# Performance work log

Hardware: AMD Instinct MI355X
Metric: run time of the kernel (lower is better)

## Reference

```python
import jax, jax.numpy as jnp
import numpy as np

N = 50000          # total nodes
B = 10             # graphs in batch
NPG = N // B       # nodes per graph (equal-sized graphs)
E = 800000         # edges
IN_DIM = 128
HID = 128
NHEAD = 4
DHEAD = HID // NHEAD
T = 1000
SLOPE = 0.2        # leaky_relu negative slope
ALPHA_L = 2.0


def _ln(x, g=None, b=None, eps=1e-5):
    mu = jnp.mean(x, axis=-1, keepdims=True)
    var = jnp.var(x, axis=-1, keepdims=True)
    y = (x - mu) * jax.lax.rsqrt(var + eps)
    if g is not None:
        y = y * g + b
    return y


def _gatv2(h, src, dst, Ws, Wd, a, b):
    # DGL GATv2Conv, share_weights=False, residual=False, bias=True, activation=gelu
    fs = (h @ Ws).reshape(N, NHEAD, DHEAD)
    fd = (h @ Wd).reshape(N, NHEAD, DHEAD)
    # per-edge attention logits [E, NHEAD]
    e = jnp.sum(jax.nn.leaky_relu(fs[src] + fd[dst], SLOPE) * a, axis=-1)
    # edge softmax grouped by destination node
    m = jax.ops.segment_max(e, dst, num_segments=N)
    ee = jnp.exp(e - m[dst])
    den = jax.ops.segment_sum(ee, dst, num_segments=N)
    alpha = ee / den[dst]                                  # [E, NHEAD]
    rst = jax.ops.segment_sum(alpha[..., None] * fs[src], dst, num_segments=N)
    rst = jax.nn.gelu(rst + b.reshape(1, NHEAD, DHEAD), approximate=False)
    return rst.reshape(N, HID)


def _forward(x, noise, sab, somab, time_emb,
             Ws0, Wd0, a0, b0, g0, be0,
             Ws1, Wd1, a1, b1, g1, be1,
             Wo1, bo1, Wo2, bo2, src, dst, t):
    # sample_q: statistics-matched signed noise
    miu = jnp.mean(x, axis=0)
    std = jnp.std(x, axis=0, ddof=1)          # torch.std is unbiased
    nz = _ln(noise) * std + miu
    nz = jnp.sign(x) * jnp.abs(nz)
    s1 = jnp.repeat(sab[t], NPG)[:, None]
    s2 = jnp.repeat(somab[t], NPG)[:, None]
    x_t = s1 * x + s2 * nz
    temb = jnp.repeat(time_emb[t], NPG, axis=0)
    # Denoising_Unet
    h = jnp.concatenate([x_t, temb], axis=1)   # [N, IN_DIM+HID]
    h = _ln(_gatv2(h, src, dst, Ws0, Wd0, a0, b0), g0, be0)
    h_in = h
    h = _gatv2(h, src, dst, Ws1, Wd1, a1, b1)
    h = _ln(h + h_in, g1, be1)                 # residual (shapes match)
    out = jax.nn.relu(h @ Wo1 + bo1) @ Wo2 + bo2
    # loss_fn
    mse = jnp.mean((out - x) ** 2)
    on = out / jnp.maximum(jnp.linalg.norm(out, axis=-1, keepdims=True), 1e-12)
    xn = x / jnp.maximum(jnp.linalg.norm(x, axis=-1, keepdims=True), 1e-12)
    cos = jnp.mean((1.0 - jnp.sum(on * xn, axis=-1)) ** ALPHA_L)
    return mse + 0.1 * cos


def setup_inputs() -> dict:
    key = jax.random.key(0)
    ks = jax.random.split(key, 26)
    betas = np.linspace(1e-4, 0.02, T, dtype=np.float64)
    ab = np.cumprod(1.0 - betas)
    s = 0.02
    in0 = IN_DIM + HID
    inp = {}
    inp['x'] = jax.random.normal(ks[0], (N, IN_DIM), jnp.float32)
    inp['noise'] = jax.random.normal(ks[1], (N, IN_DIM), jnp.float32)
    inp['src'] = jax.random.randint(ks[2], (E,), 0, N, dtype=jnp.int32)
    inp['dst'] = jax.random.randint(ks[3], (E,), 0, N, dtype=jnp.int32)
    inp['t'] = jax.random.randint(ks[4], (B,), 0, T, dtype=jnp.int32)
    inp['sab'] = jnp.asarray(np.sqrt(ab), jnp.float32)
    inp['somab'] = jnp.asarray(np.sqrt(1.0 - ab), jnp.float32)
    inp['time_emb'] = jax.random.normal(ks[5], (T, HID), jnp.float32) * s
    inp['Ws0'] = jax.random.normal(ks[6], (in0, HID), jnp.float32) * s
    inp['Wd0'] = jax.random.normal(ks[7], (in0, HID), jnp.float32) * s
    inp['a0'] = jax.random.normal(ks[8], (NHEAD, DHEAD), jnp.float32) * s
    inp['b0'] = jnp.zeros((HID,), jnp.float32)
    inp['g0'] = jnp.ones((HID,), jnp.float32)
    inp['be0'] = jnp.zeros((HID,), jnp.float32)
    inp['Ws1'] = jax.random.normal(ks[9], (HID, HID), jnp.float32) * s
    inp['Wd1'] = jax.random.normal(ks[10], (HID, HID), jnp.float32) * s
    inp['a1'] = jax.random.normal(ks[11], (NHEAD, DHEAD), jnp.float32) * s
    inp['b1'] = jnp.zeros((HID,), jnp.float32)
    inp['g1'] = jnp.ones((HID,), jnp.float32)
    inp['be1'] = jnp.zeros((HID,), jnp.float32)
    inp['Wo1'] = jax.random.normal(ks[12], (HID, HID), jnp.float32) * s
    inp['bo1'] = jnp.zeros((HID,), jnp.float32)
    inp['Wo2'] = jax.random.normal(ks[13], (HID, IN_DIM), jnp.float32) * s
    inp['bo2'] = jnp.zeros((IN_DIM,), jnp.float32)
    return inp


def reference(x, noise, src, dst, t, sab, somab, time_emb,
              Ws0, Wd0, a0, b0, g0, be0,
              Ws1, Wd1, a1, b1, g1, be1,
              Wo1, bo1, Wo2, bo2):
    return _forward(x, noise, sab, somab, time_emb,
                    Ws0, Wd0, a0, b0, g0, be0,
                    Ws1, Wd1, a1, b1, g1, be1,
                    Wo1, bo1, Wo2, bo2, src, dst, t)
```

## Files before the change

### kernel.cpp

```cpp
#include <hip/hip_runtime.h>
#include <hip/hip_bf16.h>
#include <math.h>

#define NN 50000
#define EE 800000
#define NPG 5000

typedef short bf16x8 __attribute__((ext_vector_type(8)));
typedef float f32x4 __attribute__((ext_vector_type(4)));

__device__ __forceinline__ float gelu_exact(float v) {
    return 0.5f * v * (1.0f + erff(v * 0.70710678118654752440f));
}

__device__ __forceinline__ ushort f2b(float f) {
    union { float f; uint u; } v; v.f = f;
    uint r = (v.u + 0x7fffu + ((v.u >> 16) & 1)) >> 16;
    return (ushort)r;
}
__device__ __forceinline__ uint pack2(float a, float b) {
    return (uint)f2b(a) | ((uint)f2b(b) << 16);
}
__device__ __forceinline__ float blo(uint u) {
    union { uint u; float f; } v; v.u = u << 16; return v.f;
}
__device__ __forceinline__ float bhi(uint u) {
    union { uint u; float f; } v; v.u = u & 0xffff0000u; return v.f;
}

__global__ void probe_kernel(int* sink) {
    if (blockIdx.x == 99999) sink[0] = 1;
}

__global__ __launch_bounds__(256) void colstats_kernel(const float* __restrict__ x,
                                                       float* __restrict__ sums, int n) {
    int tid = threadIdx.x;
    int col4 = (tid & 31) * 4;
    int rowgrp = tid >> 5;
    float s0 = 0.f, s1 = 0.f, s2 = 0.f, s3 = 0.f;
    float q0 = 0.f, q1 = 0.f, q2 = 0.f, q3 = 0.f;
    for (int r = blockIdx.x * 8 + rowgrp; r < n; r += gridDim.x * 8) {
        float4 v = *(const float4*)(x + (size_t)r * 128 + col4);
        s0 += v.x; s1 += v.y; s2 += v.z; s3 += v.w;
        q0 += v.x * v.x; q1 += v.y * v.y; q2 += v.z * v.z; q3 += v.w * v.w;
    }
    s0 += __shfl_xor(s0, 32); s1 += __shfl_xor(s1, 32);
    s2 += __shfl_xor(s2, 32); s3 += __shfl_xor(s3, 32);
    q0 += __shfl_xor(q0, 32); q1 += __shfl_xor(q1, 32);
    q2 += __shfl_xor(q2, 32); q3 += __shfl_xor(q3, 32);
    __shared__ float red[4][32][8];
    int wv = tid >> 6, l = tid & 63;
    if (l < 32) {
        float* p = red[wv][l];
        p[0] = s0; p[1] = s1; p[2] = s2; p[3] = s3;
        p[4] = q0; p[5] = q1; p[6] = q2; p[7] = q3;
    }
    __syncthreads();
    if (tid < 32) {
        float a0 = 0.f, a1 = 0.f, a2 = 0.f, a3 = 0.f;
        float b0 = 0.f, b1 = 0.f, b2 = 0.f, b3 = 0.f;
#pragma unroll
        for (int w = 0; w < 4; ++w) {
            float* p = red[w][tid];
            a0 += p[0]; a1 += p[1]; a2 += p[2]; a3 += p[3];
            b0 += p[4]; b1 += p[5]; b2 += p[6]; b3 += p[7];
        }
        int c = tid * 4;
        atomicAdd(&sums[c], a0); atomicAdd(&sums[c + 1], a1);
        atomicAdd(&sums[c + 2], a2); atomicAdd(&sums[c + 3], a3);
        atomicAdd(&sums[128 + c], b0); atomicAdd(&sums[128 + c + 1], b1);
        atomicAdd(&sums[128 + c + 2], b2); atomicAdd(&sums[128 + c + 3], b3);
    }
}

__global__ void finalize_stats_kernel(float* __restrict__ stats, int n) {
    int c = threadIdx.x;
    float sum = stats[c], sumsq = stats[128 + c];
    float mu = sum / (float)n;
    float var = (sumsq - sum * sum / (float)n) / (float)(n - 1);
    stats[256 + c] = mu;
    stats[384 + c] = sqrtf(fmaxf(var, 0.f));
}

__global__ __launch_bounds__(256) void build_h_kernel(const float* __restrict__ x,
        const float* __restrict__ noise, const int* __restrict__ t,
        const float* __restrict__ sab, const float* __restrict__ somab,
        const float* __restrict__ temb, const float* __restrict__ stats,
        ushort* __restrict__ h, int n) {
    int wid = (blockIdx.x * blockDim.x + threadIdx.x) >> 6;
    int lane = threadIdx.x & 63;
    if (wid >= n) return;
    int tt = t[wid / NPG];
    float s1 = sab[tt], s2v = somab[tt];
    float2 nz = ((const float2*)noise)[(size_t)wid * 64 + lane];
    float s = nz.x + nz.y;
    float sq = nz.x * nz.x + nz.y * nz.y;
#pragma unroll
    for (int o = 1; o < 64; o <<= 1) { s += __shfl_xor(s, o); sq += __shfl_xor(sq, o); }
    float mu = s * (1.f / 128.f);
    float var = sq * (1.f / 128.f) - mu * mu;
    float r = rsqrtf(var + 1e-5f);
    int f0 = 2 * lane, f1 = f0 + 1;
    float y0 = (nz.x - mu) * r * stats[384 + f0] + stats[256 + f0];
    float y1 = (nz.y - mu) * r * stats[384 + f1] + stats[256 + f1];
    float2 xv = ((const float2*)x)[(size_t)wid * 64 + lane];
    float sg0 = (xv.x > 0.f) ? 1.f : ((xv.x < 0.f) ? -1.f : 0.f);
    float sg1 = (xv.y > 0.f) ? 1.f : ((xv.y < 0.f) ? -1.f : 0.f);
    float n0 = sg0 * fabsf(y0);
    float n1 = sg1 * fabsf(y1);
    float xt0 = s1 * xv.x + s2v * n0;
    float xt1 = s1 * xv.y + s2v * n1;
    uint* row = (uint*)(h + (size_t)wid * 256);
    row[lane] = pack2(xt0, xt1);
    float2 te = ((const float2*)(temb + (size_t)tt * 128))[lane];
    row[64 + lane] = pack2(te.x, te.y);
}

__global__ __launch_bounds__(256) void convert_weights(const float* __restrict__ Ws0,
        const float* __restrict__ Wd0, const float* __restrict__ Ws1,
        const float* __restrict__ Wd1, const float* __restrict__ Wo1,
        const float* __restrict__ Wo2, ushort* __restrict__ Wt0,
        ushort* __restrict__ Wt1, ushort* __restrict__ Wo1t, ushort* __restrict__ Wo2t) {
    int i = blockIdx.x * 256 + threadIdx.x;
    if (i < 65536) {
        int c = i >> 8, k = i & 255;
        const float* W = (c < 128) ? Ws0 : Wd0;
        Wt0[c * 256 + k] = f2b(W[k * 128 + (c & 127)]);
    } else if (i < 98304) {
        int j = i - 65536;
        int c = j >> 7, k = j & 127;
        const float* W = (c < 128) ? Ws1 : Wd1;
        Wt1[c * 128 + k] = f2b(W[k * 128 + (c & 127)]);
    } else if (i < 114688) {
        int j = i - 98304;
        int c = j >> 7, k = j & 127;
        Wo1t[c * 128 + k] = f2b(Wo1[k * 128 + c]);
    } else if (i < 131072) {
        int j = i - 114688;
        int c = j >> 7, k = j & 127;
        Wo2t[c * 128 + k] = f2b(Wo2[k * 128 + c]);
    }
}

__global__ void hist_kernel(const int* __restrict__ dst, int* __restrict__ counts, int e) {
    int i = blockIdx.x * blockDim.x + threadIdx.x;
    if (i < e) atomicAdd(&counts[dst[i]], 1);
}

__global__ __launch_bounds__(1024) void scan_reduce_kernel(const int* __restrict__ counts,
        int* __restrict__ blockSums, int n) {
    int i = blockIdx.x * 1024 + threadIdx.x;
    int v = (i < n) ? counts[i] : 0;
#pragma unroll
    for (int o = 32; o > 0; o >>= 1) v += __shfl_down(v, o);
    __shared__ int sh[16];
    int lane = threadIdx.x & 63, wv = threadIdx.x >> 6;
    if (lane == 0) sh[wv] = v;
    __syncthreads();
    if (threadIdx.x == 0) {
        int s = 0;
#pragma unroll
        for (int k = 0; k < 16; ++k) s += sh[k];
        blockSums[blockIdx.x] = s;
    }
}

__global__ __launch_bounds__(64) void scan_offsets_kernel(const int* __restrict__ blockSums,
        int* __restrict__ blockOffs, int* __restrict__ indptr, int nb, int n) {
    int tid = threadIdx.x;
    int v = (tid < nb) ? blockSums[tid] : 0;
    int incl = v;
#pragma unroll
    for (int o = 1; o < 64; o <<= 1) {
        int tv = __shfl_up(incl, o);
        if (tid >= o) incl += tv;
    }
    if (tid < nb) blockOffs[tid] = incl - v;
    if (tid == 63) indptr[n] = incl;
}

__global__ __launch_bounds__(1024) void scan_apply_kernel(const int* __restrict__ counts,
        const int* __restrict__ blockOffs, int* __restrict__ indptr,
        int* __restrict__ cursor, int n) {
    int tid = threadIdx.x;
    int i = blockIdx.x * 1024 + tid;
    int v = (i < n) ? counts[i] : 0;
    int lane = tid & 63, wv = tid >> 6;
    int incl = v;
#pragma unroll
    for (int o = 1; o < 64; o <<= 1) {
        int tv = __shfl_up(incl, o);
        if (lane >= o) incl += tv;
    }
    __shared__ int wsum[16];
    __shared__ int woff[16];
    if (lane == 63) wsum[wv] = incl;
    __syncthreads();
    if (tid == 0) {
        int s = 0;
#pragma unroll
        for (int k = 0; k < 16; ++k) { woff[k] = s; s += wsum[k]; }
    }
    __syncthreads();
    int ex = incl - v + woff[wv] + blockOffs[blockIdx.x];
    if (i < n) { indptr[i] = ex; cursor[i] = ex; }
}

__global__ void scatter_kernel(const int* __restrict__ src, const int* __restrict__ dst,
                               int* __restrict__ cursor, int* __restrict__ csr_src, int e) {
    int i = blockIdx.x * blockDim.x + threadIdx.x;
    if (i < e) {
        int p = atomicAdd(&cursor[dst[i]], 1);
        csr_src[p] = src[i];
    }
}

template<int K, int EPI>
__global__ __launch_bounds__(256, 2) void gemm_resW(const ushort* __restrict__ A,
        const ushort* __restrict__ Wt, const float* __restrict__ bias,
        ushort* __restrict__ C0, float* __restrict__ Cf, int M) {
    constexpr int K2 = K * 2;
    __shared__ ushort Wl[128 * K];
    int tid = threadIdx.x;
    int wave = tid >> 6, lane = tid & 63;
    int l15 = lane & 15, g = lane >> 4;

#pragma unroll
    for (int it = 0; it < K / 16; ++it) {
        int q = (it * 256 + tid) * 16;
        int col = q / K2, qk = q % K2;
        int srcb = col * K2 + (qk ^ ((col & 7) << 4));
        *(float4*)((char*)Wl + q) = *(const float4*)((const char*)Wt + srcb);
    }
    __syncthreads();

    int rowBase = blockIdx.x * 256 + wave * 64;
    f32x4 acc[4][8] = {};

#pragma unroll
    for (int ks = 0; ks < K / 32; ++ks) {
        bf16x8 af[4];
#pragma unroll
        for (int fr = 0; fr < 4; ++fr) {
            int row = rowBase + fr * 16 + l15;
            int rc = min(row, M - 1);
            af[fr] = *(const bf16x8*)(A + (size_t)rc * K + ks * 32 + g * 8);
        }
#pragma unroll
        for (int n = 0; n < 8; ++n) {
            int col = n * 16 + l15;
            int boff = col * K2 + (((ks * 64 + g * 16)) ^ ((col & 7) << 4));
            bf16x8 bf = *(const bf16x8*)((const char*)Wl + boff);
#pragma unroll
            for (int fr = 0; fr < 4; ++fr)
                acc[fr][n] = __builtin_amdgcn_mfma_f32_16x16x32_bf16(af[fr], bf, acc[fr][n], 0, 0, 0);
        }
    }

#pragma unroll
    for (int fr = 0; fr < 4; ++fr) {
#pragma unroll
        for (int n = 0; n < 8; ++n) {
            int col = n * 16 + l15;
#pragma unroll
            for (int j = 0; j < 4; ++j) {
                int row = rowBase + fr * 16 + g * 4 + j;
                if (row < M) {
                    float v = acc[fr][n][j];
                    if (EPI == 1) v = fmaxf(v + bias[col], 0.f);
                    if (EPI == 2) v = v + bias[col];
                    if (EPI == 2) Cf[(size_t)row * 128 + col] = v;
                    else          C0[(size_t)row * 128 + col] = f2b(v);
                }
            }
        }
    }
}

__global__ __launch_bounds__(256) void gat_ln_kernel(const ushort* __restrict__ fs,
        const ushort* __restrict__ fd, const float* __restrict__ a,
        const float* __restrict__ bias, const int* __restrict__ indptr,
        const int* __restrict__ csr_src, const float* __restrict__ resid,
        const float* __restrict__ g, const float* __restrict__ be,
        float* __restrict__ outF, ushort* __restrict__ outB, int n) {
    int wid = (blockIdx.x * blockDim.x + threadIdx.x) >> 6;
    int lane = threadIdx.x & 63;
    if (wid >= n) return;
    int beg = indptr[wid], cnt = indptr[wid + 1] - beg;
    const int* ip = csr_src + beg;
    uint fdu = ((const uint*)fd)[(size_t)wid * 64 + lane];
    float fd0 = blo(fdu), fd1 = bhi(fdu);
    float a0 = a[2 * lane], a1 = a[2 * lane + 1];
    const uint* fsu = (const uint*)fs;
    float den = 0.f, acc0 = 0.f, acc1 = 0.f;
    int s0 = (0 < cnt) ? ip[0] : 0;
    int s1 = (1 < cnt) ? ip[1] : 0;
    int s2 = (2 < cnt) ? ip[2] : 0;
    int s3 = (3 < cnt) ? ip[3] : 0;
    uint v0 = fsu[(size_t)s0 * 64 + lane];
    uint v1 = fsu[(size_t)s1 * 64 + lane];
    uint v2 = fsu[(size_t)s2 * 64 + lane];
    uint v3 = fsu[(size_t)s3 * 64 + lane];
    int i0 = (4 < cnt) ? ip[4] : 0;
    int i1 = (5 < cnt) ? ip[5] : 0;
    int i2 = (6 < cnt) ? ip[6] : 0;
    int i3 = (7 < cnt) ? ip[7] : 0;
    for (int j = 0; j < cnt; ++j) {
        uint cur = v0;
        v0 = v1; v1 = v2; v2 = v3;
        v3 = fsu[(size_t)i0 * 64 + lane];
        i0 = i1; i1 = i2; i2 = i3;
        i3 = (j + 8 < cnt) ? ip[j + 8] : 0;
        float c0 = blo(cur), c1 = bhi(cur);
        float t0 = c0 + fd0; t0 = (t0 > 0.f ? t0 : 0.2f * t0) * a0;
        float t1 = c1 + fd1; t1 = (t1 > 0.f ? t1 : 0.2f * t1) * a1;
        float p = t0 + t1;
        p += __shfl_xor(p, 1); p += __shfl_xor(p, 2);
        p += __shfl_xor(p, 4); p += __shfl_xor(p, 8);
        float w = __expf(p);
        den += w;
        acc0 = fmaf(w, c0, acc0);
        acc1 = fmaf(w, c1, acc1);
    }
    float inv = (cnt > 0) ? 1.f / den : 0.f;
    float r0 = gelu_exact(acc0 * inv + bias[2 * lane]);
    float r1 = gelu_exact(acc1 * inv + bias[2 * lane + 1]);
    if (resid) {
        float2 rr = ((const float2*)resid)[(size_t)wid * 64 + lane];
        r0 += rr.x; r1 += rr.y;
    }
    float s = r0 + r1;
    float sq = r0 * r0 + r1 * r1;
#pragma unroll
    for (int o = 1; o < 64; o <<= 1) { s += __shfl_xor(s, o); sq += __shfl_xor(sq, o); }
    float mu = s * (1.f / 128.f);
    float var = sq * (1.f / 128.f) - mu * mu;
    float rstd = rsqrtf(var + 1e-5f);
    float2 gg = ((const float2*)g)[lane];
    float2 bb = ((const float2*)be)[lane];
    float o0 = (r0 - mu) * rstd * gg.x + bb.x;
    float o1 = (r1 - mu) * rstd * gg.y + bb.y;
    if (outF) ((float2*)outF)[(size_t)wid * 64 + lane] = make_float2(o0, o1);
    if (outB) ((uint*)outB)[(size_t)wid * 64 + lane] = pack2(o0, o1);
}

__global__ __launch_bounds__(256) void loss_partial_kernel(const float* __restrict__ out,
        const float* __restrict__ x, float* __restrict__ partials, int n) {
    __shared__ float sm[8];
    int lane = threadIdx.x & 63;
    int wv = threadIdx.x >> 6;
    int gw = blockIdx.x * 4 + wv;
    float d2 = 0.f, closs = 0.f;
    for (int row = gw; row < n; row += 4096) {
        float2 o = ((const float2*)out)[(size_t)row * 64 + lane];
        float2 xv = ((const float2*)x)[(size_t)row * 64 + lane];
        float e0 = o.x - xv.x, e1 = o.y - xv.y;
        d2 += e0 * e0 + e1 * e1;
        float oo = o.x * o.x + o.y * o.y;
        float xx = xv.x * xv.x + xv.y * xv.y;
        float ox = o.x * xv.x + o.y * xv.y;
#pragma unroll
        for (int s = 1; s < 64; s <<= 1) {
            oo += __shfl_xor(oo, s); xx += __shfl_xor(xx, s); ox += __shfl_xor(ox, s);
        }
        float no = fmaxf(sqrtf(oo), 1e-12f);
        float nx = fmaxf(sqrtf(xx), 1e-12f);
        float cs = 1.f - ox / (no * nx);
        closs += cs * cs;
    }
#pragma unroll
    for (int s = 1; s < 64; s <<= 1) d2 += __shfl_xor(d2, s);
    if (lane == 0) { sm[wv] = d2; sm[4 + wv] = closs; }
    __syncthreads();
    if (threadIdx.x == 0) {
        partials[2 * blockIdx.x] = sm[0] + sm[1] + sm[2] + sm[3];
        partials[2 * blockIdx.x + 1] = sm[4] + sm[5] + sm[6] + sm[7];
    }
}

__global__ __launch_bounds__(1024) void loss_final_kernel(const float* __restrict__ partials,
        float* __restrict__ outp, int nb, int n) {
    __shared__ double sd[32];
    int tid = threadIdx.x;
    double m = 0.0, c = 0.0;
    for (int i = tid; i < nb; i += 1024) { m += partials[2 * i]; c += partials[2 * i + 1]; }
#pragma unroll
    for (int s = 1; s < 64; s <<= 1) { m += __shfl_xor(m, s); c += __shfl_xor(c, s); }
    int wv = tid >> 6, lane = tid & 63;
    if (lane == 0) { sd[wv] = m; sd[16 + wv] = c; }
    __syncthreads();
    if (tid == 0) {
        double mt = 0.0, ct = 0.0;
        for (int i = 0; i < 16; ++i) { mt += sd[i]; ct += sd[16 + i]; }
        outp[0] = (float)(mt / ((double)n * 128.0) + 0.1 * ct / (double)n);
    }
}

extern "C" void kernel_launch(void* const* d_in, const int* in_sizes, int n_in,
                              void* d_out, int out_size, void* d_ws, size_t ws_size,
                              hipStream_t stream) {
    const int N = NN, E = EE;
    const float* x     = (const float*)d_in[0];
    const float* noise = (const float*)d_in[1];
    const int*   src   = (const int*)d_in[2];
    const int*   dst   = (const int*)d_in[3];
    const int*   t     = (const int*)d_in[4];
    const float* sab   = (const float*)d_in[5];
    const float* somab = (const float*)d_in[6];
    const float* temb  = (const float*)d_in[7];
    const float* Ws0   = (const float*)d_in[8];
    const float* Wd0   = (const float*)d_in[9];
    const float* a0    = (const float*)d_in[10];
    const float* b0    = (const float*)d_in[11];
    const float* g0    = (const float*)d_in[12];
    const float* be0   = (const float*)d_in[13];
    const float* Ws1   = (const float*)d_in[14];
    const float* Wd1   = (const float*)d_in[15];
    const float* a1    = (const float*)d_in[16];
    const float* b1    = (const float*)d_in[17];
    const float* g1    = (const float*)d_in[18];
    const float* be1   = (const float*)d_in[19];
    const float* Wo1   = (const float*)d_in[20];
    const float* bo1   = (const float*)d_in[21];
    const float* Wo2   = (const float*)d_in[22];
    const float* bo2   = (const float*)d_in[23];

    float* ws = (float*)d_ws;
    ushort* hB  = (ushort*)ws;
    ushort* Pb  = (ushort*)ws;
    ushort* fsB = (ushort*)(ws + (size_t)N * 128);
    ushort* fdB = (ushort*)(ws + (size_t)N * 192);
    float*  P   = ws + (size_t)N * 256;
    float*  outb = P;
    ushort* Qb  = fdB;
    ushort* z   = fsB;
    float* wtail = ws + (size_t)N * 384;
    ushort* Wt0  = (ushort*)wtail;
    ushort* Wt1  = (ushort*)(wtail + 32768);
    ushort* Wo1t = (ushort*)(wtail + 49152);
    ushort* Wo2t = (ushort*)(wtail + 57344);
    float* stats    = wtail + 65536;
    float* partials = stats + 512;
    int* counts  = (int*)(partials + 2048);
    int* indptr  = counts + N;
    int* cursor  = indptr + N + 1;
    int* csr_src = cursor + N;
    int* blockSums = csr_src + E;
    int* blockOffs = blockSums + 64;

    probe_kernel<<<256, 64, 0, stream>>>(blockSums);

    hipMemsetAsync(stats, 0, 512 * sizeof(float), stream);
    hipMemsetAsync(counts, 0, (size_t)N * sizeof(int), stream);

    colstats_kernel<<<1024, 256, 0, stream>>>(x, stats, N);
    finalize_stats_kernel<<<1, 128, 0, stream>>>(stats, N);
    build_h_kernel<<<(N + 3) / 4, 256, 0, stream>>>(x, noise, t, sab, somab, temb, stats, hB, N);
    convert_weights<<<512, 256, 0, stream>>>(Ws0, Wd0, Ws1, Wd1, Wo1, Wo2, Wt0, Wt1, Wo1t, Wo2t);

    hist_kernel<<<(E + 255) / 256, 256, 0, stream>>>(dst, counts, E);
    int nScanB = (N + 1023) / 1024;
    scan_reduce_kernel<<<nScanB, 1024, 0, stream>>>(counts, blockSums, N);
    scan_offsets_kernel<<<1, 64, 0, stream>>>(blockSums, blockOffs, indptr, nScanB, N);
    scan_apply_kernel<<<nScanB, 1024, 0, stream>>>(counts, blockOffs, indptr, cursor, N);
    scatter_kernel<<<(E + 255) / 256, 256, 0, stream>>>(src, dst, cursor, csr_src, E);

    int gemmGrid = (N + 255) / 256;
    gemm_resW<256, 0><<<gemmGrid, 256, 0, stream>>>(hB, Wt0, nullptr, fsB, nullptr, N);
    gemm_resW<256, 0><<<gemmGrid, 256, 0, stream>>>(hB, Wt0 + 128 * 256, nullptr, fdB, nullptr, N);
    gat_ln_kernel<<<(N + 3) / 4, 256, 0, stream>>>(fsB, fdB, a0, b0, indptr, csr_src,
                                                   nullptr, g0, be0, P, Pb, N);
    gemm_resW<128, 0><<<gemmGrid, 256, 0, stream>>>(Pb, Wt1, nullptr, fsB, nullptr, N);
    gemm_resW<128, 0><<<gemmGrid, 256, 0, stream>>>(Pb, Wt1 + 128 * 128, nullptr, fdB, nullptr, N);
    gat_ln_kernel<<<(N + 3) / 4, 256, 0, stream>>>(fsB, fdB, a1, b1, indptr, csr_src,
                                                   P, g1, be1, nullptr, Qb, N);
    gemm_resW<128, 1><<<gemmGrid, 256, 0, stream>>>(Qb, Wo1t, bo1, z, nullptr, N);
    gemm_resW<128, 2><<<gemmGrid, 256, 0, stream>>>(z, Wo2t, bo2, nullptr, outb, N);

    loss_partial_kernel<<<1024, 256, 0, stream>>>(outb, x, partials, N);
    loss_final_kernel<<<1, 1024, 0, stream>>>(partials, (float*)d_out, 1024, N);
}
```

Measured before the change: 473.7 us.

## Merge preprocessing kernels, batch paired GEMMs, split GAT edges across two waves

Folds column stats, histogram and weight conversion into one launch, then merges the stats finalize with the scan reduce, and the h build with the scan apply. This cuts kernel launches and drops the probe kernel. The fs/fd GEMM pairs now run as one launch each by selecting weights and outputs per block. The GAT aggregation splits each node's edges across two waves with a deeper gather prefetch and combines the partial sums through shared memory. The trade-off is an extra block-wide sync in the GAT kernel and more register pressure from the 8-deep prefetch.

```diff
diff --git a/kernel.cpp b/kernel.cpp
--- a/kernel.cpp
+++ b/kernel.cpp
@@ -28,187 +28,190 @@
     union { uint u; float f; } v; v.u = u & 0xffff0000u; return v.f;
 }
 
-__global__ void probe_kernel(int* sink) {
-    if (blockIdx.x == 99999) sink[0] = 1;
-}
-
-__global__ __launch_bounds__(256) void colstats_kernel(const float* __restrict__ x,
-                                                       float* __restrict__ sums, int n) {
+__global__ __launch_bounds__(256) void head1_kernel(const float* __restrict__ x,
+        float* __restrict__ sums, const int* __restrict__ dst, int* __restrict__ counts,
+        const float* __restrict__ Ws0, const float* __restrict__ Wd0,
+        const float* __restrict__ Ws1, const float* __restrict__ Wd1,
+        const float* __restrict__ Wo1, const float* __restrict__ Wo2,
+        ushort* __restrict__ Wt0, ushort* __restrict__ Wt1,
+        ushort* __restrict__ Wo1t, ushort* __restrict__ Wo2t) {
+    int bid = blockIdx.x;
     int tid = threadIdx.x;
-    int col4 = (tid & 31) * 4;
-    int rowgrp = tid >> 5;
-    float s0 = 0.f, s1 = 0.f, s2 = 0.f, s3 = 0.f;
-    float q0 = 0.f, q1 = 0.f, q2 = 0.f, q3 = 0.f;
-    for (int r = blockIdx.x * 8 + rowgrp; r < n; r += gridDim.x * 8) {
-        float4 v = *(const float4*)(x + (size_t)r * 128 + col4);
-        s0 += v.x; s1 += v.y; s2 += v.z; s3 += v.w;
-        q0 += v.x * v.x; q1 += v.y * v.y; q2 += v.z * v.z; q3 += v.w * v.w;
-    }
-    s0 += __shfl_xor(s0, 32); s1 += __shfl_xor(s1, 32);
-    s2 += __shfl_xor(s2, 32); s3 += __shfl_xor(s3, 32);
-    q0 += __shfl_xor(q0, 32); q1 += __shfl_xor(q1, 32);
-    q2 += __shfl_xor(q2, 32); q3 += __shfl_xor(q3, 32);
-    __shared__ float red[4][32][8];
-    int wv = tid >> 6, l = tid & 63;
-    if (l < 32) {
-        float* p = red[wv][l];
-        p[0] = s0; p[1] = s1; p[2] = s2; p[3] = s3;
-        p[4] = q0; p[5] = q1; p[6] = q2; p[7] = q3;
-    }
-    __syncthreads();
-    if (tid < 32) {
-        float a0 = 0.f, a1 = 0.f, a2 = 0.f, a3 = 0.f;
-        float b0 = 0.f, b1 = 0.f, b2 = 0.f, b3 = 0.f;
-#pragma unroll
-        for (int w = 0; w < 4; ++w) {
-            float* p = red[w][tid];
-            a0 += p[0]; a1 += p[1]; a2 += p[2]; a3 += p[3];
-            b0 += p[4]; b1 += p[5]; b2 += p[6]; b3 += p[7];
-        }
-        int c = tid * 4;
-        atomicAdd(&sums[c], a0); atomicAdd(&sums[c + 1], a1);
-        atomicAdd(&sums[c + 2], a2); atomicAdd(&sums[c + 3], a3);
-        atomicAdd(&sums[128 + c], b0); atomicAdd(&sums[128 + c + 1], b1);
-        atomicAdd(&sums[128 + c + 2], b2); atomicAdd(&sums[128 + c + 3], b3);
-    }
-}
-
-__global__ void finalize_stats_kernel(float* __restrict__ stats, int n) {
-    int c = threadIdx.x;
-    float sum = stats[c], sumsq = stats[128 + c];
-    float mu = sum / (float)n;
-    float var = (sumsq - sum * sum / (float)n) / (float)(n - 1);
-    stats[256 + c] = mu;
-    stats[384 + c] = sqrtf(fmaxf(var, 0.f));
-}
-
-__global__ __launch_bounds__(256) void build_h_kernel(const float* __restrict__ x,
+    if (bid < 1024) {
+        int col4 = (tid & 31) * 4;
+        int rowgrp = tid >> 5;
+        float s0 = 0.f, s1 = 0.f, s2 = 0.f, s3 = 0.f;
+        float q0 = 0.f, q1 = 0.f, q2 = 0.f, q3 = 0.f;
+        for (int r = bid * 8 + rowgrp; r < NN; r += 8192) {
+            float4 v = *(const float4*)(x + (size_t)r * 128 + col4);
+            s0 += v.x; s1 += v.y; s2 += v.z; s3 += v.w;
+            q0 += v.x * v.x; q1 += v.y * v.y; q2 += v.z * v.z; q3 += v.w * v.w;
+        }
+        s0 += __shfl_xor(s0, 32); s1 += __shfl_xor(s1, 32);
+        s2 += __shfl_xor(s2, 32); s3 += __shfl_xor(s3, 32);
+        q0 += __shfl_xor(q0, 32); q1 += __shfl_xor(q1, 32);
+        q2 += __shfl_xor(q2, 32); q3 += __shfl_xor(q3, 32);
+        __shared__ float red[4][32][8];
+        int wv = tid >> 6, l = tid & 63;
+        if (l < 32) {
+            float* p = red[wv][l];
+            p[0] = s0; p[1] = s1; p[2] = s2; p[3] = s3;
+            p[4] = q0; p[5] = q1; p[6] = q2; p[7] = q3;
+        }
+        __syncthreads();
+        if (tid < 32) {
+            float a0 = 0.f, a1 = 0.f, a2 = 0.f, a3 = 0.f;
+            float b0 = 0.f, b1 = 0.f, b2 = 0.f, b3 = 0.f;
+#pragma unroll
+            for (int w = 0; w < 4; ++w) {
+                float* p = red[w][tid];
+                a0 += p[0]; a1 += p[1]; a2 += p[2]; a3 += p[3];
+                b0 += p[4]; b1 += p[5]; b2 += p[6]; b3 += p[7];
+            }
+            int c = tid * 4;
+            atomicAdd(&sums[c], a0); atomicAdd(&sums[c + 1], a1);
+            atomicAdd(&sums[c + 2], a2); atomicAdd(&sums[c + 3], a3);
+            atomicAdd(&sums[128 + c], b0); atomicAdd(&sums[128 + c + 1], b1);
+            atomicAdd(&sums[128 + c + 2], b2); atomicAdd(&sums[128 + c + 3], b3);
+        }
+    } else if (bid < 4149) {
+        int i = (bid - 1024) * 256 + tid;
+        if (i < EE) atomicAdd(&counts[dst[i]], 1);
+    } else {
+        int i = (bid - 4149) * 256 + tid;
+        if (i < 65536) {
+            int c = i >> 8, k = i & 255;
+            const float* W = (c < 128) ? Ws0 : Wd0;
+            Wt0[c * 256 + k] = f2b(W[k * 128 + (c & 127)]);
+        } else if (i < 98304) {
+            int j = i - 65536;
+            int c = j >> 7, k = j & 127;
+            const float* W = (c < 128) ? Ws1 : Wd1;
+            Wt1[c * 128 + k] = f2b(W[k * 128 + (c & 127)]);
+        } else if (i < 114688) {
+            int j = i - 98304;
+            int c = j >> 7, k = j & 127;
+            Wo1t[c * 128 + k] = f2b(Wo1[k * 128 + c]);
+        } else if (i < 131072) {
+            int j = i - 114688;
+            int c = j >> 7, k = j & 127;
+            Wo2t[c * 128 + k] = f2b(Wo2[k * 128 + c]);
+        }
+    }
+}
+
+__global__ __launch_bounds__(1024) void head2_kernel(const int* __restrict__ counts,
+        int* __restrict__ blockSums, float* __restrict__ stats, int n) {
+    int bid = blockIdx.x;
+    int tid = threadIdx.x;
+    if (bid < 49) {
+        int i = bid * 1024 + tid;
+        int v = (i < n) ? counts[i] : 0;
+#pragma unroll
+        for (int o = 32; o > 0; o >>= 1) v += __shfl_down(v, o);
+        __shared__ int sh[16];
+        int lane = tid & 63, wv = tid >> 6;
+        if (lane == 0) sh[wv] = v;
+        __syncthreads();
+        if (tid == 0) {
+            int s = 0;
+#pragma unroll
+            for (int k = 0; k < 16; ++k) s += sh[k];
+            blockSums[bid] = s;
+        }
+    } else {
+        if (tid < 128) {
+            int c = tid;
+            float sum = stats[c], sumsq = stats[128 + c];
+            float mu = sum / (float)n;
+            float var = (sumsq - sum * sum / (float)n) / (float)(n - 1);
+            stats[256 + c] = mu;
+            stats[384 + c] = sqrtf(fmaxf(var, 0.f));
+        }
+    }
+}
+
+__global__ __launch_bounds__(1024) void head3_kernel(const float* __restrict__ x,
         const float* __restrict__ noise, const int* __restrict__ t,
         const float* __restrict__ sab, const float* __restrict__ somab,
         const float* __restrict__ temb, const float* __restrict__ stats,
-        ushort* __restrict__ h, int n) {
-    int wid = (blockIdx.x * blockDim.x + threadIdx.x) >> 6;
-    int lane = threadIdx.x & 63;
-    if (wid >= n) return;
-    int tt = t[wid / NPG];
-    float s1 = sab[tt], s2v = somab[tt];
-    float2 nz = ((const float2*)noise)[(size_t)wid * 64 + lane];
-    float s = nz.x + nz.y;
-    float sq = nz.x * nz.x + nz.y * nz.y;
-#pragma unroll
-    for (int o = 1; o < 64; o <<= 1) { s += __shfl_xor(s, o); sq += __shfl_xor(sq, o); }
-    float mu = s * (1.f / 128.f);
-    float var = sq * (1.f / 128.f) - mu * mu;
-    float r = rsqrtf(var + 1e-5f);
-    int f0 = 2 * lane, f1 = f0 + 1;
-    float y0 = (nz.x - mu) * r * stats[384 + f0] + stats[256 + f0];
-    float y1 = (nz.y - mu) * r * stats[384 + f1] + stats[256 + f1];
-    float2 xv = ((const float2*)x)[(size_t)wid * 64 + lane];
-    float sg0 = (xv.x > 0.f) ? 1.f : ((xv.x < 0.f) ? -1.f : 0.f);
-    float sg1 = (xv.y > 0.f) ? 1.f : ((xv.y < 0.f) ? -1.f : 0.f);
-    float n0 = sg0 * fabsf(y0);
-    float n1 = sg1 * fabsf(y1);
-    float xt0 = s1 * xv.x + s2v * n0;
-    float xt1 = s1 * xv.y + s2v * n1;
-    uint* row = (uint*)(h + (size_t)wid * 256);
-    row[lane] = pack2(xt0, xt1);
-    float2 te = ((const float2*)(temb + (size_t)tt * 128))[lane];
-    row[64 + lane] = pack2(te.x, te.y);
-}
-
-__global__ __launch_bounds__(256) void convert_weights(const float* __restrict__ Ws0,
-        const float* __restrict__ Wd0, const float* __restrict__ Ws1,
-        const float* __restrict__ Wd1, const float* __restrict__ Wo1,
-        const float* __restrict__ Wo2, ushort* __restrict__ Wt0,
-        ushort* __restrict__ Wt1, ushort* __restrict__ Wo1t, ushort* __restrict__ Wo2t) {
-    int i = blockIdx.x * 256 + threadIdx.x;
-    if (i < 65536) {
-        int c = i >> 8, k = i & 255;
-        const float* W = (c < 128) ? Ws0 : Wd0;
-        Wt0[c * 256 + k] = f2b(W[k * 128 + (c & 127)]);
-    } else if (i < 98304) {
-        int j = i - 65536;
-        int c = j >> 7, k = j & 127;
-        const float* W = (c < 128) ? Ws1 : Wd1;
-        Wt1[c * 128 + k] = f2b(W[k * 128 + (c & 127)]);
-    } else if (i < 114688) {
-        int j = i - 98304;
-        int c = j >> 7, k = j & 127;
-        Wo1t[c * 128 + k] = f2b(Wo1[k * 128 + c]);
-    } else if (i < 131072) {
-        int j = i - 114688;
-        int c = j >> 7, k = j & 127;
-        Wo2t[c * 128 + k] = f2b(Wo2[k * 128 + c]);
-    }
-}
-
-__global__ void hist_kernel(const int* __restrict__ dst, int* __restrict__ counts, int e) {
-    int i = blockIdx.x * blockDim.x + threadIdx.x;
-    if (i < e) atomicAdd(&counts[dst[i]], 1);
-}
-
-__global__ __launch_bounds__(1024) void scan_reduce_kernel(const int* __restrict__ counts,
-        int* __restrict__ blockSums, int n) {
+        ushort* __restrict__ h,
+        const int* __restrict__ counts, const int* __restrict__ blockSums,
+        int* __restrict__ indptr, int* __restrict__ cursor, int n) {
+    int bid = blockIdx.x;
+    int tid = threadIdx.x;
+    if (bid < 3125) {
+        int wid = bid * 16 + (tid >> 6);
+        int lane = tid & 63;
+        int tt = t[wid / NPG];
+        float s1 = sab[tt], s2v = somab[tt];
+        float2 nz = ((const float2*)noise)[(size_t)wid * 64 + lane];
+        float s = nz.x + nz.y;
+        float sq = nz.x * nz.x + nz.y * nz.y;
+#pragma unroll
+        for (int o = 1; o < 64; o <<= 1) { s += __shfl_xor(s, o); sq += __shfl_xor(sq, o); }
+        float mu = s * (1.f / 128.f);
+        float var = sq * (1.f / 128.f) - mu * mu;
+        float r = rsqrtf(var + 1e-5f);
+        int f0 = 2 * lane, f1 = f0 + 1;
+        float y0 = (nz.x - mu) * r * stats[384 + f0] + stats[256 + f0];
+        float y1 = (nz.y - mu) * r * stats[384 + f1] + stats[256 + f1];
+        float2 xv = ((const float2*)x)[(size_t)wid * 64 + lane];
+        float sg0 = (xv.x > 0.f) ? 1.f : ((xv.x < 0.f) ? -1.f : 0.f);
+        float sg1 = (xv.y > 0.f) ? 1.f : ((xv.y < 0.f) ? -1.f : 0.f);
+        float n0 = sg0 * fabsf(y0);
+        float n1 = sg1 * fabsf(y1);
+        float xt0 = s1 * xv.x + s2v * n0;
+        float xt1 = s1 * xv.y + s2v * n1;
+        uint* row = (uint*)(h + (size_t)wid * 256);
+        row[lane] = pack2(xt0, xt1);
+        float2 te = ((const float2*)(temb + (size_t)tt * 128))[lane];
+        row[64 + lane] = pack2(te.x, te.y);
+    } else {
+        int b = bid - 3125;
+        __shared__ int sOff, sTot;
+        if (tid < 64) {
+            int v = (tid < 49) ? blockSums[tid] : 0;
+            int incl = v;
+#pragma unroll
+            for (int o = 1; o < 64; o <<= 1) {
+                int tv = __shfl_up(incl, o);
+                if ((tid & 63) >= o) incl += tv;
+            }
+            int off = (b == 0) ? 0 : __shfl(incl, b - 1);
+            int tot = __shfl(incl, 48);
+            if (tid == 0) { sOff = off; sTot = tot; }
+        }
+        __syncthreads();
+        int i = b * 1024 + tid;
+        int v = (i < n) ? counts[i] : 0;
+        int lane = tid & 63, wv = tid >> 6;
+        int incl = v;
+#pragma unroll
+        for (int o = 1; o < 64; o <<= 1) {
+            int tv = __shfl_up(incl, o);
+            if (lane >= o) incl += tv;
+        }
+        __shared__ int wsum[16];
+        __shared__ int woff[16];
+        if (lane == 63) wsum[wv] = incl;
+        __syncthreads();
+        if (tid == 0) {
+            int s = 0;
+#pragma unroll
+            for (int k = 0; k < 16; ++k) { woff[k] = s; s += wsum[k]; }
+        }
+        __syncthreads();
+        int ex = incl - v + woff[wv] + sOff;
+        if (i < n) { indptr[i] = ex; cursor[i] = ex; }
+        if (b == 48 && tid == 0) indptr[n] = sTot;
+    }
+}
+
+__global__ __launch_bounds__(1024) void scatter_kernel(const int* __restrict__ src,
+        const int* __restrict__ dst, int* __restrict__ cursor,
+        int* __restrict__ csr_src, int e) {
     int i = blockIdx.x * 1024 + threadIdx.x;
-    int v = (i < n) ? counts[i] : 0;
-#pragma unroll
-    for (int o = 32; o > 0; o >>= 1) v += __shfl_down(v, o);
-    __shared__ int sh[16];
-    int lane = threadIdx.x & 63, wv = threadIdx.x >> 6;
-    if (lane == 0) sh[wv] = v;
-    __syncthreads();
-    if (threadIdx.x == 0) {
-        int s = 0;
-#pragma unroll
-        for (int k = 0; k < 16; ++k) s += sh[k];
-        blockSums[blockIdx.x] = s;
-    }
-}
-
-__global__ __launch_bounds__(64) void scan_offsets_kernel(const int* __restrict__ blockSums,
-        int* __restrict__ blockOffs, int* __restrict__ indptr, int nb, int n) {
-    int tid = threadIdx.x;
-    int v = (tid < nb) ? blockSums[tid] : 0;
-    int incl = v;
-#pragma unroll
-    for (int o = 1; o < 64; o <<= 1) {
-        int tv = __shfl_up(incl, o);
-        if (tid >= o) incl += tv;
-    }
-    if (tid < nb) blockOffs[tid] = incl - v;
-    if (tid == 63) indptr[n] = incl;
-}
-
-__global__ __launch_bounds__(1024) void scan_apply_kernel(const int* __restrict__ counts,
-        const int* __restrict__ blockOffs, int* __restrict__ indptr,
-        int* __restrict__ cursor, int n) {
-    int tid = threadIdx.x;
-    int i = blockIdx.x * 1024 + tid;
-    int v = (i < n) ? counts[i] : 0;
-    int lane = tid & 63, wv = tid >> 6;
-    int incl = v;
-#pragma unroll
-    for (int o = 1; o < 64; o <<= 1) {
-        int tv = __shfl_up(incl, o);
-        if (lane >= o) incl += tv;
-    }
-    __shared__ int wsum[16];
-    __shared__ int woff[16];
-    if (lane == 63) wsum[wv] = incl;
-    __syncthreads();
-    if (tid == 0) {
-        int s = 0;
-#pragma unroll
-        for (int k = 0; k < 16; ++k) { woff[k] = s; s += wsum[k]; }
-    }
-    __syncthreads();
-    int ex = incl - v + woff[wv] + blockOffs[blockIdx.x];
-    if (i < n) { indptr[i] = ex; cursor[i] = ex; }
-}
-
-__global__ void scatter_kernel(const int* __restrict__ src, const int* __restrict__ dst,
-                               int* __restrict__ cursor, int* __restrict__ csr_src, int e) {
-    int i = blockIdx.x * blockDim.x + threadIdx.x;
     if (i < e) {
         int p = atomicAdd(&cursor[dst[i]], 1);
         csr_src[p] = src[i];
@@ -217,13 +220,19 @@
 
 template<int K, int EPI>
 __global__ __launch_bounds__(256, 2) void gemm_resW(const ushort* __restrict__ A,
-        const ushort* __restrict__ Wt, const float* __restrict__ bias,
-        ushort* __restrict__ C0, float* __restrict__ Cf, int M) {
+        const ushort* __restrict__ WtA, const ushort* __restrict__ WtB,
+        const float* __restrict__ bias,
+        ushort* __restrict__ outA, ushort* __restrict__ outB,
+        float* __restrict__ Cf, int half, int M) {
     constexpr int K2 = K * 2;
     __shared__ ushort Wl[128 * K];
     int tid = threadIdx.x;
     int wave = tid >> 6, lane = tid & 63;
     int l15 = lane & 15, g = lane >> 4;
+    bool isB = blockIdx.x >= half;
+    const ushort* Wt = isB ? WtB : WtA;
+    ushort* C0 = isB ? outB : outA;
+    int mb = isB ? (blockIdx.x - half) : blockIdx.x;
 
 #pragma unroll
     for (int it = 0; it < K / 16; ++it) {
@@ -234,7 +243,7 @@
     }
     __syncthreads();
 
-    int rowBase = blockIdx.x * 256 + wave * 64;
+    int rowBase = mb * 256 + wave * 64;
     f32x4 acc[4][8] = {};
 
 #pragma unroll
@@ -249,7 +258,7 @@
 #pragma unroll
         for (int n = 0; n < 8; ++n) {
             int col = n * 16 + l15;
-            int boff = col * K2 + (((ks * 64 + g * 16)) ^ ((col & 7) << 4));
+            int boff = col * K2 + ((ks * 64 + g * 16) ^ ((col & 7) << 4));
             bf16x8 bf = *(const bf16x8*)((const char*)Wl + boff);
 #pragma unroll
             for (int fr = 0; fr < 4; ++fr)
@@ -283,65 +292,91 @@
         const int* __restrict__ csr_src, const float* __restrict__ resid,
         const float* __restrict__ g, const float* __restrict__ be,
         float* __restrict__ outF, ushort* __restrict__ outB, int n) {
-    int wid = (blockIdx.x * blockDim.x + threadIdx.x) >> 6;
-    int lane = threadIdx.x & 63;
-    if (wid >= n) return;
-    int beg = indptr[wid], cnt = indptr[wid + 1] - beg;
-    const int* ip = csr_src + beg;
+    int tid = threadIdx.x;
+    int wave = tid >> 6, lane = tid & 63;
+    int nodeLocal = wave >> 1;
+    int half = wave & 1;
+    int wid = blockIdx.x * 2 + nodeLocal;
+    int beg = indptr[wid], end = indptr[wid + 1];
+    int cnt = end - beg;
+    int c0 = (cnt + 1) >> 1;
+    int myBeg = beg + (half ? c0 : 0);
+    int myCnt = half ? (cnt - c0) : c0;
+    const int* ip = csr_src + myBeg;
+
     uint fdu = ((const uint*)fd)[(size_t)wid * 64 + lane];
     float fd0 = blo(fdu), fd1 = bhi(fdu);
     float a0 = a[2 * lane], a1 = a[2 * lane + 1];
     const uint* fsu = (const uint*)fs;
+
+    int e0 = (0 < myCnt) ? ip[0] : 0;
+    int e1 = (1 < myCnt) ? ip[1] : 0;
+    int e2 = (2 < myCnt) ? ip[2] : 0;
+    int e3 = (3 < myCnt) ? ip[3] : 0;
+    int e4 = (4 < myCnt) ? ip[4] : 0;
+    int e5 = (5 < myCnt) ? ip[5] : 0;
+    int e6 = (6 < myCnt) ? ip[6] : 0;
+    int e7 = (7 < myCnt) ? ip[7] : 0;
+    uint v0 = fsu[(size_t)e0 * 64 + lane];
+    uint v1 = fsu[(size_t)e1 * 64 + lane];
+    uint v2 = fsu[(size_t)e2 * 64 + lane];
+    uint v3 = fsu[(size_t)e3 * 64 + lane];
+    uint v4 = fsu[(size_t)e4 * 64 + lane];
+    uint v5 = fsu[(size_t)e5 * 64 + lane];
+    uint v6 = fsu[(size_t)e6 * 64 + lane];
+    uint v7 = fsu[(size_t)e7 * 64 + lane];
+
     float den = 0.f, acc0 = 0.f, acc1 = 0.f;
-    int s0 = (0 < cnt) ? ip[0] : 0;
-    int s1 = (1 < cnt) ? ip[1] : 0;
-    int s2 = (2 < cnt) ? ip[2] : 0;
-    int s3 = (3 < cnt) ? ip[3] : 0;
-    uint v0 = fsu[(size_t)s0 * 64 + lane];
-    uint v1 = fsu[(size_t)s1 * 64 + lane];
-    uint v2 = fsu[(size_t)s2 * 64 + lane];
-    uint v3 = fsu[(size_t)s3 * 64 + lane];
-    int i0 = (4 < cnt) ? ip[4] : 0;
-    int i1 = (5 < cnt) ? ip[5] : 0;
-    int i2 = (6 < cnt) ? ip[6] : 0;
-    int i3 = (7 < cnt) ? ip[7] : 0;
-    for (int j = 0; j < cnt; ++j) {
+#pragma unroll 4
+    for (int j = 0; j < myCnt; ++j) {
         uint cur = v0;
-        v0 = v1; v1 = v2; v2 = v3;
-        v3 = fsu[(size_t)i0 * 64 + lane];
-        i0 = i1; i1 = i2; i2 = i3;
-        i3 = (j + 8 < cnt) ? ip[j + 8] : 0;
-        float c0 = blo(cur), c1 = bhi(cur);
-        float t0 = c0 + fd0; t0 = (t0 > 0.f ? t0 : 0.2f * t0) * a0;
-        float t1 = c1 + fd1; t1 = (t1 > 0.f ? t1 : 0.2f * t1) * a1;
+        v0 = v1; v1 = v2; v2 = v3; v3 = v4; v4 = v5; v5 = v6; v6 = v7;
+        int nj = j + 8;
+        int ni = (nj < myCnt) ? ip[nj] : 0;
+        v7 = fsu[(size_t)ni * 64 + lane];
+        float c0f = blo(cur), c1f = bhi(cur);
+        float t0 = c0f + fd0; t0 = (t0 > 0.f ? t0 : 0.2f * t0) * a0;
+        float t1 = c1f + fd1; t1 = (t1 > 0.f ? t1 : 0.2f * t1) * a1;
         float p = t0 + t1;
         p += __shfl_xor(p, 1); p += __shfl_xor(p, 2);
         p += __shfl_xor(p, 4); p += __shfl_xor(p, 8);
         float w = __expf(p);
         den += w;
-        acc0 = fmaf(w, c0, acc0);
-        acc1 = fmaf(w, c1, acc1);
-    }
-    float inv = (cnt > 0) ? 1.f / den : 0.f;
-    float r0 = gelu_exact(acc0 * inv + bias[2 * lane]);
-    float r1 = gelu_exact(acc1 * inv + bias[2 * lane + 1]);
-    if (resid) {
-        float2 rr = ((const float2*)resid)[(size_t)wid * 64 + lane];
-        r0 += rr.x; r1 += rr.y;
-    }
-    float s = r0 + r1;
-    float sq = r0 * r0 + r1 * r1;
-#pragma unroll
-    for (int o = 1; o < 64; o <<= 1) { s += __shfl_xor(s, o); sq += __shfl_xor(sq, o); }
-    float mu = s * (1.f / 128.f);
-    float var = sq * (1.f / 128.f) - mu * mu;
-    float rstd = rsqrtf(var + 1e-5f);
-    float2 gg = ((const float2*)g)[lane];
-    float2 bb = ((const float2*)be)[lane];
-    float o0 = (r0 - mu) * rstd * gg.x + bb.x;
-    float o1 = (r1 - mu) * rstd * gg.y + bb.y;
-    if (outF) ((float2*)outF)[(size_t)wid * 64 + lane] = make_float2(o0, o1);
-    if (outB) ((uint*)outB)[(size_t)wid * 64 + lane] = pack2(o0, o1);
+        acc0 = fmaf(w, c0f, acc0);
+        acc1 = fmaf(w, c1f, acc1);
+    }
+
+    __shared__ float sAcc[4][64][2];
+    __shared__ float sDen[4][64];
+    sAcc[wave][lane][0] = acc0;
+    sAcc[wave][lane][1] = acc1;
+    sDen[wave][lane] = den;
+    __syncthreads();
+    if (half == 0) {
+        acc0 += sAcc[wave + 1][lane][0];
+        acc1 += sAcc[wave + 1][lane][1];
+        den  += sDen[wave + 1][lane];
+        float inv = (cnt > 0) ? 1.f / den : 0.f;
+        float r0 = gelu_exact(acc0 * inv + bias[2 * lane]);
+        float r1 = gelu_exact(acc1 * inv + bias[2 * lane + 1]);
+        if (resid) {
+            float2 rr = ((const float2*)resid)[(size_t)wid * 64 + lane];
+            r0 += rr.x; r1 += rr.y;
+        }
+        float s = r0 + r1;
+        float sq = r0 * r0 + r1 * r1;
+#pragma unroll
+        for (int o = 1; o < 64; o <<= 1) { s += __shfl_xor(s, o); sq += __shfl_xor(sq, o); }
+        float mu = s * (1.f / 128.f);
+        float var = sq * (1.f / 128.f) - mu * mu;
+        float rstd = rsqrtf(var + 1e-5f);
+        float2 gg = ((const float2*)g)[lane];
+        float2 bb = ((const float2*)be)[lane];
+        float o0 = (r0 - mu) * rstd * gg.x + bb.x;
+        float o1 = (r1 - mu) * rstd * gg.y + bb.y;
+        if (outF) ((float2*)outF)[(size_t)wid * 64 + lane] = make_float2(o0, o1);
+        if (outB) ((uint*)outB)[(size_t)wid * 64 + lane] = pack2(o0, o1);
+    }
 }
 
 __global__ __launch_bounds__(256) void loss_partial_kernel(const float* __restrict__ out,
@@ -446,36 +481,30 @@
     int* cursor  = indptr + N + 1;
     int* csr_src = cursor + N;
     int* blockSums = csr_src + E;
-    int* blockOffs = blockSums + 64;
-
-    probe_kernel<<<256, 64, 0, stream>>>(blockSums);
 
     hipMemsetAsync(stats, 0, 512 * sizeof(float), stream);
     hipMemsetAsync(counts, 0, (size_t)N * sizeof(int), stream);
 
-    colstats_kernel<<<1024, 256, 0, stream>>>(x, stats, N);
-    finalize_stats_kernel<<<1, 128, 0, stream>>>(stats, N);
-    build_h_kernel<<<(N + 3) / 4, 256, 0, stream>>>(x, noise, t, sab, somab, temb, stats, hB, N);
-    convert_weights<<<512, 256, 0, stream>>>(Ws0, Wd0, Ws1, Wd1, Wo1, Wo2, Wt0, Wt1, Wo1t, Wo2t);
-
-    hist_kernel<<<(E + 255) / 256, 256, 0, stream>>>(dst, counts, E);
-    int nScanB = (N + 1023) / 1024;
-    scan_reduce_kernel<<<nScanB, 1024, 0, stream>>>(counts, blockSums, N);
-    scan_offsets_kernel<<<1, 64, 0, stream>>>(blockSums, blockOffs, indptr, nScanB, N);
-    scan_apply_kernel<<<nScanB, 1024, 0, stream>>>(counts, blockOffs, indptr, cursor, N);
-    scatter_kernel<<<(E + 255) / 256, 256, 0, stream>>>(src, dst, cursor, csr_src, E);
-
-    int gemmGrid = (N + 255) / 256;
-    gemm_resW<256, 0><<<gemmGrid, 256, 0, stream>>>(hB, Wt0, nullptr, fsB, nullptr, N);
-    gemm_resW<256, 0><<<gemmGrid, 256, 0, stream>>>(hB, Wt0 + 128 * 256, nullptr, fdB, nullptr, N);
-    gat_ln_kernel<<<(N + 3) / 4, 256, 0, stream>>>(fsB, fdB, a0, b0, indptr, csr_src,
-                                                   nullptr, g0, be0, P, Pb, N);
-    gemm_resW<128, 0><<<gemmGrid, 256, 0, stream>>>(Pb, Wt1, nullptr, fsB, nullptr, N);
-    gemm_resW<128, 0><<<gemmGrid, 256, 0, stream>>>(Pb, Wt1 + 128 * 128, nullptr, fdB, nullptr, N);
-    gat_ln_kernel<<<(N + 3) / 4, 256, 0, stream>>>(fsB, fdB, a1, b1, indptr, csr_src,
-                                                   P, g1, be1, nullptr, Qb, N);
-    gemm_resW<128, 1><<<gemmGrid, 256, 0, stream>>>(Qb, Wo1t, bo1, z, nullptr, N);
-    gemm_resW<128, 2><<<gemmGrid, 256, 0, stream>>>(z, Wo2t, bo2, nullptr, outb, N);
+    head1_kernel<<<4661, 256, 0, stream>>>(x, stats, dst, counts,
+                                           Ws0, Wd0, Ws1, Wd1, Wo1, Wo2,
+                                           Wt0, Wt1, Wo1t, Wo2t);
+    head2_kernel<<<50, 1024, 0, stream>>>(counts, blockSums, stats, N);
+    head3_kernel<<<3174, 1024, 0, stream>>>(x, noise, t, sab, somab, temb, stats, hB,
+                                            counts, blockSums, indptr, cursor, N);
+    scatter_kernel<<<(E + 1023) / 1024, 1024, 0, stream>>>(src, dst, cursor, csr_src, E);
+
+    gemm_resW<256, 0><<<392, 256, 0, stream>>>(hB, Wt0, Wt0 + 128 * 256, nullptr,
+                                               fsB, fdB, nullptr, 196, N);
+    gat_ln_kernel<<<N / 2, 256, 0, stream>>>(fsB, fdB, a0, b0, indptr, csr_src,
+                                             nullptr, g0, be0, P, Pb, N);
+    gemm_resW<128, 0><<<392, 256, 0, stream>>>(Pb, Wt1, Wt1 + 128 * 128, nullptr,
+                                               fsB, fdB, nullptr, 196, N);
+    gat_ln_kernel<<<N / 2, 256, 0, stream>>>(fsB, fdB, a1, b1, indptr, csr_src,
+                                             P, g1, be1, nullptr, Qb, N);
+    gemm_resW<128, 1><<<196, 256, 0, stream>>>(Qb, Wo1t, Wo1t, bo1,
+                                               z, z, nullptr, 196, N);
+    gemm_resW<128, 2><<<196, 256, 0, stream>>>(z, Wo2t, Wo2t, bo2,
+                                               nullptr, nullptr, outb, 196, N);
 
     loss_partial_kernel<<<1024, 256, 0, stream>>>(outb, x, partials, N);
     loss_final_kernel<<<1, 1024, 0, stream>>>(partials, (float*)d_out, 1024, N);
```

After: 479.2 us. Within noise of the previous version (+1.2%).
